# Optimization experiments

Measured on AMD Instinct MI355X. Metric: run time of the kernel, lower is better.

Reference implementation:

```python
import jax, jax.numpy as jnp
import numpy as np
from jax import lax

DILATIONS = (1, 3, 9, 27, 81, 1)
C = 128        # model channels
UP = 2048      # up-projection channels
K = 512        # filterbank kernel size
NZ = 64        # non_zero_elements kept by sparsify
B = 2
N = 32768      # n_samples


def conv1d(x, w, b, dilation=1, padding='VALID'):
    # x: [B,Cin,T], w: [Cout,Cin,Kw]
    y = lax.conv_general_dilated(x, w, (1,), padding, rhs_dilation=(dilation,),
                                 dimension_numbers=('NCH', 'OIH', 'NCH'))
    return y if b is None else y + b[None, :, None]


def dilated_stack(x, ws, bs, causal_past):
    # residual stack of kernel-2 dilated causal convs; 'only-past' pads left, 'only-future' pads right
    for i, d in enumerate(DILATIONS):
        pad = ((0, 0), (0, 0), (d, 0)) if causal_past else ((0, 0), (0, 0), (0, d))
        h = conv1d(jnp.pad(x, pad), ws[i], bs[i], dilation=d)
        x = x + jax.nn.leaky_relu(h, 0.2)
    return x


def sparsify_topk(x, k):
    # keep top-k values (soft=True: keep magnitudes) over flattened (C,T) per sample
    b = x.shape[0]
    flat = x.reshape(b, -1)
    vals, idx = lax.top_k(flat, k)
    out = jnp.zeros_like(flat).at[jnp.arange(b)[:, None], idx].set(vals)
    return out.reshape(x.shape)


def setup_inputs() -> dict:
    key = jax.random.key(0)
    ks = jax.random.split(key, 11)
    s = 0.1  # weight_init
    return {
        'x': jax.random.normal(ks[0], (B, 1, N), jnp.float32),
        'fb': jax.random.normal(ks[1], (C, 1, K), jnp.float32) * s,        # filterbank
        'enc_w': jax.random.normal(ks[2], (6, C, C, 2), jnp.float32) * s,
        'enc_b': jnp.zeros((6, C), jnp.float32),
        'up_w': jax.random.normal(ks[3], (UP, C, 1), jnp.float32) * s,
        'up_b': jnp.zeros((UP,), jnp.float32),
        'down_w': jax.random.normal(ks[4], (C, UP, 1), jnp.float32) * s,
        'down_b': jnp.zeros((C,), jnp.float32),
        'dec_w': jax.random.normal(ks[5], (6, C, C, 2), jnp.float32) * s,
        'dec_b': jnp.zeros((6, C), jnp.float32),
    }


def reference(x, fb, enc_w, enc_b, up_w, up_b, down_w, down_b, dec_w, dec_b):
    # filterbank analysis: [B,1,N] -> [B,C,N]
    spec = conv1d(x, fb, None, 1, ((K // 2, K // 2 - 1),))
    enc = dilated_stack(spec, enc_w, enc_b, causal_past=False)  # 'only-future'
    enc = conv1d(enc, up_w, up_b)            # [B,2048,N]
    enc = sparsify_topk(enc, NZ)             # 64 nonzeros per sample
    enc = conv1d(enc, down_w, down_b)        # [B,128,N]
    dec = dilated_stack(enc, dec_w, dec_b, causal_past=True)    # 'only-past'
    dec = jnp.pad(dec, ((0, 0), (0, 0), (0, 1)))                # F.pad(decoded, (0,1))
    # transposed convolve back to waveform: flipped filterbank, sum over channels
    kt = jnp.flip(fb, -1).transpose(1, 0, 2)  # [1,C,K]
    final = conv1d(dec, kt, None, 1, ((K // 2 - 1, K // 2),))[:, :, :N]
    return final
```

## Files before the change

### kernel.cpp

```cpp
#include <hip/hip_runtime.h>
#include <stdint.h>

#define NB  2
#define NC  128
#define NT  32768
#define KFB 512
#define NUP 2048
#define CAP 14336

typedef unsigned int u32;
typedef unsigned short u16;
typedef short s16;
typedef float f32x4 __attribute__((ext_vector_type(4)));
typedef s16 short8 __attribute__((ext_vector_type(8)));
typedef u32 u32x4 __attribute__((ext_vector_type(4)));

__device__ __forceinline__ u32 f2key(float v){
  u32 u = __float_as_uint(v);
  return (u & 0x80000000u) ? ~u : (u | 0x80000000u);
}
__device__ __forceinline__ float key2f(u32 k){
  u32 u = (k & 0x80000000u) ? (k & 0x7FFFFFFFu) : ~k;
  return __uint_as_float(u);
}
__device__ __forceinline__ u16 bf16rn(float v){
  u32 u = __float_as_uint(v);
  return (u16)((u + 0x7FFFu + ((u>>16)&1u)) >> 16);
}
__device__ __forceinline__ u32 packhl(float v){
  u16 h = bf16rn(v);
  u16 lo = bf16rn(v - __uint_as_float(((u32)h)<<16));
  return ((u32)h<<16) | lo;
}
__device__ __forceinline__ void unpack8(const u32* p, short8& xh, short8& xl){
  u32x4 r0 = *(const u32x4*)p;
  u32x4 r1 = *(const u32x4*)(p + 4);
  union { u32 u[4]; short8 v; } H, L;
  H.u[0] = __builtin_amdgcn_perm(r0.y, r0.x, 0x07060302u);
  H.u[1] = __builtin_amdgcn_perm(r0.w, r0.z, 0x07060302u);
  H.u[2] = __builtin_amdgcn_perm(r1.y, r1.x, 0x07060302u);
  H.u[3] = __builtin_amdgcn_perm(r1.w, r1.z, 0x07060302u);
  L.u[0] = __builtin_amdgcn_perm(r0.y, r0.x, 0x05040100u);
  L.u[1] = __builtin_amdgcn_perm(r0.w, r0.z, 0x05040100u);
  L.u[2] = __builtin_amdgcn_perm(r1.y, r1.x, 0x05040100u);
  L.u[3] = __builtin_amdgcn_perm(r1.w, r1.z, 0x05040100u);
  xh = H.v; xl = L.v;
}

#define RS 132

__global__ __launch_bounds__(256) void k_prep(const float* __restrict__ encw,
    const float* __restrict__ decw, const float* __restrict__ upw,
    const float* __restrict__ fbw,
    u16* __restrict__ wdil, u16* __restrict__ wup, u16* __restrict__ wfb,
    u32* __restrict__ h1, u32* __restrict__ h2, int* __restrict__ counts){
  int g = blockIdx.x*256 + threadIdx.x;
  if (g < 2048) h1[g] = 0u;
  else if (g < 4096) h2[g-2048] = 0u;
  if (g < NB) counts[g] = 0;
  if (g < 49152){
    int l = g & 63, mt = (g>>6)&7, s = (g>>9)&7, layer = g>>12;
    const float* W = (layer < 6) ? (encw + (size_t)layer*NC*NC*2)
                                 : (decw + (size_t)(layer-6)*NC*NC*2);
    int co = mt*16 + (l & 15);
    int kb = s*32 + ((l>>4)<<3);
    union { u16 h[8]; u32x4 q; } H, L;
    #pragma unroll
    for (int j=0;j<8;++j){
      int k = kb + j;
      float v = W[((size_t)co*NC + (k&127))*2 + (k>>7)];
      u16 h = bf16rn(v);
      H.h[j] = h;
      L.h[j] = bf16rn(v - __uint_as_float(((u32)h)<<16));
    }
    int unit = g >> 6;
    *(u32x4*)(wdil + (size_t)unit*1024 + (l<<3)) = H.q;
    *(u32x4*)(wdil + (size_t)unit*1024 + 512 + (l<<3)) = L.q;
  } else if (g < 81920){
    int g2 = g - 49152;
    int l = g2 & 63, umt = (g2>>6)&127, s = g2>>13;
    int u = umt*16 + (l & 15);
    int kb = s*32 + ((l>>4)<<3);
    union { u16 h[8]; u32x4 q; } H, L;
    #pragma unroll
    for (int j=0;j<8;++j){
      float v = upw[(size_t)u*NC + kb + j];
      u16 h = bf16rn(v);
      H.h[j] = h;
      L.h[j] = bf16rn(v - __uint_as_float(((u32)h)<<16));
    }
    int unit = g2 >> 6;
    *(u32x4*)(wup + (size_t)unit*1024 + (l<<3)) = H.q;
    *(u32x4*)(wup + (size_t)unit*1024 + 512 + (l<<3)) = L.q;
  } else if (g < 90112){
    int g3 = g - 81920;
    int l = g3 & 63, mt = (g3>>6)&7, s = g3>>9;
    int c = mt*16 + (l & 15);
    int kb = s*32 + ((l>>4)<<3);
    union { u16 h[8]; u32x4 q; } H, L;
    #pragma unroll
    for (int j=0;j<8;++j){
      float v = fbw[(size_t)c*KFB + kb + j];
      u16 h = bf16rn(v);
      H.h[j] = h;
      L.h[j] = bf16rn(v - __uint_as_float(((u32)h)<<16));
    }
    int unit = g3 >> 6;
    *(u32x4*)(wfb + (size_t)unit*1024 + (l<<3)) = H.q;
    *(u32x4*)(wfb + (size_t)unit*1024 + 512 + (l<<3)) = L.q;
  }
}

__global__ __launch_bounds__(256) void k_fb(const float* __restrict__ x,
    const u16* __restrict__ wfb, float* __restrict__ spec){
  __shared__ u32 xw[640];
  const int tid = threadIdx.x;
  const int t0 = blockIdx.x << 7;
  const int b  = blockIdx.y;
  const int lane = tid & 63, w = tid >> 6;
  const int wy = w >> 1, wx = w & 1;
  const int quad = lane >> 4, l15 = lane & 15;
  for (int i = tid; i < 640; i += 256){
    int t = t0 - 256 + i;
    float v = ((u32)t < (u32)NT) ? x[b*NT + t] : 0.0f;
    xw[i] = packhl(v);
  }
  __syncthreads();
  f32x4 acc[4][4] = {};
  for (int s = 0; s < 16; ++s){
    short8 ah[4], al[4];
    #pragma unroll
    for (int mt=0; mt<4; ++mt){
      const u16* p = wfb + (size_t)(s*8 + wy*4 + mt)*1024 + (lane<<3);
      ah[mt] = *(const short8*)p;
      al[mt] = *(const short8*)(p + 512);
    }
    short8 xh[4], xl[4];
    #pragma unroll
    for (int nt=0; nt<4; ++nt){
      int base = s*32 + quad*8 + (wx<<6) + (nt<<4) + l15;
      u32 r[8];
      #pragma unroll
      for (int j=0;j<8;++j) r[j] = xw[base + j];
      union { u32 u[4]; short8 v; } H, L;
      H.u[0] = __builtin_amdgcn_perm(r[1], r[0], 0x07060302u);
      H.u[1] = __builtin_amdgcn_perm(r[3], r[2], 0x07060302u);
      H.u[2] = __builtin_amdgcn_perm(r[5], r[4], 0x07060302u);
      H.u[3] = __builtin_amdgcn_perm(r[7], r[6], 0x07060302u);
      L.u[0] = __builtin_amdgcn_perm(r[1], r[0], 0x05040100u);
      L.u[1] = __builtin_amdgcn_perm(r[3], r[2], 0x05040100u);
      L.u[2] = __builtin_amdgcn_perm(r[5], r[4], 0x05040100u);
      L.u[3] = __builtin_amdgcn_perm(r[7], r[6], 0x05040100u);
      xh[nt] = H.v; xl[nt] = L.v;
    }
    #pragma unroll
    for (int mt=0; mt<4; ++mt){
      #pragma unroll
      for (int nt=0; nt<4; ++nt){
        acc[mt][nt] = __builtin_amdgcn_mfma_f32_16x16x32_bf16(ah[mt], xh[nt], acc[mt][nt], 0,0,0);
        acc[mt][nt] = __builtin_amdgcn_mfma_f32_16x16x32_bf16(ah[mt], xl[nt], acc[mt][nt], 0,0,0);
        acc[mt][nt] = __builtin_amdgcn_mfma_f32_16x16x32_bf16(al[mt], xh[nt], acc[mt][nt], 0,0,0);
      }
    }
  }
  #pragma unroll
  for (int mt=0; mt<4; ++mt){
    #pragma unroll
    for (int r=0; r<4; ++r){
      const int c = (wy<<6) + (mt<<4) + (quad<<2) + r;
      float* po = spec + (size_t)(b*NC+c)*NT + t0 + (wx<<6) + l15;
      #pragma unroll
      for (int nt=0; nt<4; ++nt) po[nt<<4] = acc[mt][nt][r];
    }
  }
}

__global__ __launch_bounds__(1024,4) void k_stack(const float* __restrict__ xin,
    float* __restrict__ xout, const u16* __restrict__ wf,
    const float* __restrict__ biases, int mode){
  extern __shared__ u32 lx[];
  const int tid = threadIdx.x;
  const int b  = blockIdx.y;
  const int T0 = blockIdx.x << 7;
  const int row0g = mode ? (T0 - 122) : T0;
  const int lane = tid & 63, w = tid >> 6;
  const int wm = w >> 2, wn = w & 3;
  const int quad = lane >> 4, l15 = lane & 15;
  {
    const float* xb = xin + (size_t)b*NC*NT;
    const int row = tid & 255;
    const int ci0 = (tid >> 8) << 5;
    const int tg = row0g + row;
    const bool ok = ((u32)tg < (u32)NT);
    const float* src = xb + (size_t)ci0*NT + tg;
    u32* dst = lx + row*RS + ci0;
    #pragma unroll
    for (int g=0; g<8; ++g){
      u32x4 q;
      #pragma unroll
      for (int k=0;k<4;++k){
        float v = ok ? src[(size_t)(g*4 + k)*NT] : 0.0f;
        q[k] = packhl(v);
      }
      *(u32x4*)(dst + g*4) = q;
    }
  }
  const int dils[6] = {1,3,9,27,81,1};
  const int Hrem[6] = {121,118,109,82,1,0};
  #pragma unroll 1
  for (int l = 0; l < 6; ++l){
    const int d = dils[l];
    const int o0 = mode ? -d : 0;
    const int o1 = mode ? 0 : d;
    const int lo = mode ? (122 - Hrem[l]) : 0;
    const int hi = mode ? 250 : (128 + Hrem[l]);
    const u16* wl = wf + ((size_t)l << 16);
    __syncthreads();
    bool act[4];
    #pragma unroll
    for (int nt=0;nt<4;++nt){
      const int Tst = (wn<<6) + (nt<<4);
      act[nt] = (Tst + 16 > lo) && (Tst < hi);
    }
    f32x4 acc[2][4] = {};
    #pragma unroll 1
    for (int s = 0; s < 8; ++s){
      short8 ah[2], al[2];
      #pragma unroll
      for (int mt=0;mt<2;++mt){
        const u16* p = wl + (size_t)(((s<<3) + (wm<<1) + mt) << 10) + (lane<<3);
        ah[mt] = *(const short8*)p;
        al[mt] = *(const short8*)(p + 512);
      }
      const int o = (s >= 4) ? o1 : o0;
      const int cig = (s & 3) << 5;
      #pragma unroll
      for (int nt=0;nt<4;++nt){
        if (!act[nt]) continue;
        const int T = ((wn<<6) + (nt<<4) + l15 + o) & 255;
        const int idx = T*RS + cig + (quad<<3);
        short8 xh, xl;
        unpack8(&lx[idx], xh, xl);
        #pragma unroll
        for (int mt=0;mt<2;++mt){
          acc[mt][nt] = __builtin_amdgcn_mfma_f32_16x16x32_bf16(ah[mt], xh, acc[mt][nt], 0,0,0);
          acc[mt][nt] = __builtin_amdgcn_mfma_f32_16x16x32_bf16(ah[mt], xl, acc[mt][nt], 0,0,0);
          acc[mt][nt] = __builtin_amdgcn_mfma_f32_16x16x32_bf16(al[mt], xh, acc[mt][nt], 0,0,0);
        }
      }
    }
    __syncthreads();
    const float* bl = biases + l*NC;
    const bool last = (l == 5);
    #pragma unroll
    for (int mt=0;mt<2;++mt){
      const int cobase = (wm<<5) + (mt<<4) + (quad<<2);
      float bv[4];
      #pragma unroll
      for (int r=0;r<4;++r) bv[r] = bl[cobase + r];
      #pragma unroll
      for (int nt=0;nt<4;++nt){
        if (!act[nt]) continue;
        const int T = (wn<<6) + (nt<<4) + l15;
        const int idx = T*RS + cobase;
        u32x4 xo = *(const u32x4*)&lx[idx];
        const int tg = row0g + T;
        const bool tvld = ((u32)tg < (u32)NT);
        float nv[4];
        #pragma unroll
        for (int r=0;r<4;++r){
          float oldv = __uint_as_float(xo[r] & 0xFFFF0000u) + __uint_as_float(xo[r] << 16);
          float h = acc[mt][nt][r] + bv[r];
          h = (h >= 0.f) ? h : 0.2f*h;
          float xn = oldv + h;
          nv[r] = tvld ? xn : 0.0f;
        }
        if (!last){
          u32x4 np;
          #pragma unroll
          for (int r=0;r<4;++r) np[r] = packhl(nv[r]);
          *(u32x4*)&lx[idx] = np;
        } else {
          const bool rowok = mode ? (T >= 122 && T < 250) : (T < 128);
          if (rowok){
            float* po = xout + (size_t)(b*NC + cobase)*NT + tg;
            #pragma unroll
            for (int r=0;r<4;++r) po[(size_t)r*NT] = nv[r];
          }
        }
      }
    }
  }
}

__global__ __launch_bounds__(256) void k_sub(const float* __restrict__ enc,
                                             const float* __restrict__ upw,
                                             const float* __restrict__ upb,
                                             u32* __restrict__ keys,
                                             u32* __restrict__ hist1){
  const int u0 = blockIdx.x * 64;
  const int i0 = blockIdx.y * 256;
  const int b  = blockIdx.z;
  __shared__ float uwl[32][68];
  __shared__ float ec[32][260];
  __shared__ u32 lh[1024];
  const int tid = threadIdx.x;
  for (int i=tid;i<1024;i+=256) lh[i] = 0u;
  const int ug = tid & 15;
  const int ig = tid >> 4;
  float acc[4][16];
  #pragma unroll
  for (int i=0;i<4;++i){
    #pragma unroll
    for (int j=0;j<16;++j) acc[i][j]=0.0f;
  }
  for (int c0=0;c0<NC;c0+=32){
    __syncthreads();
    #pragma unroll
    for (int i=0;i<8;++i){
      int flat = i*256+tid;
      uwl[flat & 31][flat >> 5] = upw[(size_t)(u0 + (flat>>5))*NC + c0 + (flat&31)];
    }
    #pragma unroll
    for (int i=0;i<32;++i){
      int flat = i*256+tid;
      ec[flat >> 8][flat & 255] = enc[(size_t)(b*NC + c0 + (flat>>8))*NT + (size_t)(i0 + (flat&255))*32];
    }
    __syncthreads();
    #pragma unroll 2
    for (int cc=0;cc<32;++cc){
      float a[4], bb[16];
      *(float4*)&a[0] = *(const float4*)&uwl[cc][ug*4];
      #pragma unroll
      for (int m=0;m<4;++m)
        *(float4*)&bb[m*4] = *(const float4*)&ec[cc][ig*16 + m*4];
      #pragma unroll
      for (int i=0;i<4;++i){
        #pragma unroll
        for (int j=0;j<16;++j)
          acc[i][j] = fmaf(a[i], bb[j], acc[i][j]);
      }
    }
  }
  #pragma unroll
  for (int i=0;i<4;++i){
    int u = u0 + ug*4 + i;
    float ub = upb[u];
    #pragma unroll
    for (int j=0;j<16;++j){
      float v = acc[i][j] + ub;
      u32 k = f2key(v);
      keys[(size_t)(b*NUP + u)*1024 + i0 + ig*16 + j] = k;
      atomicAdd(&lh[k >> 22], 1u);
    }
  }
  __syncthreads();
  for (int i=tid;i<1024;i+=256){
    u32 c = lh[i];
    if (c) atomicAdd(&hist1[b*1024 + i], c);
  }
}

__global__ __launch_bounds__(256) void k_sel(const u32* __restrict__ hist,
                                             u32* __restrict__ cstar,
                                             u32* __restrict__ nab,
                                             u32* __restrict__ t0key,
                                             int phase){
  const int b = blockIdx.x;
  __shared__ u32 s1[1024];
  __shared__ u32 s2[1024];
  __shared__ int red[256];
  const int tid = threadIdx.x;
  for (int i=tid;i<1024;i+=256) s1[i] = hist[b*1024 + i];
  __syncthreads();
  u32* cur = s1; u32* nxt = s2;
  for (int off=1; off<1024; off<<=1){
    for (int i=tid;i<1024;i+=256){
      u32 v = cur[i];
      if (i + off < 1024) v += cur[i+off];
      nxt[i] = v;
    }
    __syncthreads();
    u32* t = cur; cur = nxt; nxt = t;
  }
  u32 off0 = (phase==1) ? 0u : nab[b];
  int best = -1;
  for (int i=tid;i<1024;i+=256)
    if (off0 + cur[i] >= 64u && i > best) best = i;
  red[tid] = best;
  __syncthreads();
  for (int st=128; st>0; st>>=1){
    if (tid < st) red[tid] = max(red[tid], red[tid+st]);
    __syncthreads();
  }
  if (tid == 0){
    int bi = (red[0] < 0) ? 0 : red[0];
    if (phase == 1){
      cstar[b] = (u32)bi;
      nab[b] = (bi < 1023) ? cur[bi+1] : 0u;
    } else {
      t0key[b] = (cstar[b] << 22) | (((u32)bi) << 12);
    }
  }
}

__global__ void k_h2(const u32* __restrict__ keys, const u32* __restrict__ cstar,
                     u32* __restrict__ hist2){
  const u32 c0 = cstar[0], c1 = cstar[1];
  int i = blockIdx.x*256 + threadIdx.x;
  const int total = NB*NUP*1024;
  const int stride = gridDim.x*256;
  for (; i < total; i += stride){
    u32 k = keys[i];
    u32 cs = (i >> 21) ? c1 : c0;
    if ((k >> 22) == cs) atomicAdd(&hist2[((u32)(i>>21)<<10) + ((k>>12) & 1023u)], 1u);
  }
}

__global__ __launch_bounds__(256,2) void k_up(const float* __restrict__ enc,
    const u16* __restrict__ wf, const float* __restrict__ upb,
    const u32* __restrict__ t0key, float* __restrict__ cval,
    int* __restrict__ cidx, int* __restrict__ counts){
  extern __shared__ u32 lx[];
  const int tid = threadIdx.x;
  const int t0 = blockIdx.x << 7;
  const int b  = blockIdx.y;
  const int lane = tid & 63, w = tid >> 6;
  const int wy = w >> 1, wx = w & 1;
  const int quad = lane >> 4, l15 = lane & 15;
  {
    const float* xb = enc + (size_t)b*NC*NT + t0;
    const int row = tid >> 1;
    const int ci0 = (tid & 1) << 6;
    const float* src = xb + (size_t)ci0*NT + row;
    u32* dst = lx + row*RS + ci0;
    #pragma unroll
    for (int g=0; g<16; ++g){
      u32x4 q;
      #pragma unroll
      for (int k=0;k<4;++k) q[k] = packhl(src[(size_t)(g*4 + k)*NT]);
      *(u32x4*)(dst + g*4) = q;
    }
  }
  __syncthreads();
  float T0 = key2f(t0key[b]);
  T0 -= fabsf(T0)*3e-4f + 1e-5f;
  #pragma unroll 1
  for (int uc = 0; uc < 16; ++uc){
    f32x4 acc[4][4] = {};
    #pragma unroll 1
    for (int s = 0; s < 4; ++s){
      short8 ah[4], al[4];
      #pragma unroll
      for (int mt=0;mt<4;++mt){
        const u16* p = wf + (size_t)((s*128 + uc*8 + wy*4 + mt) << 10) + (lane<<3);
        ah[mt] = *(const short8*)p;
        al[mt] = *(const short8*)(p + 512);
      }
      const int cig = s << 5;
      #pragma unroll
      for (int nt=0;nt<4;++nt){
        const int T = (wx<<6) + (nt<<4) + l15;
        short8 xh, xl;
        unpack8(&lx[T*RS + cig + (quad<<3)], xh, xl);
        #pragma unroll
        for (int mt=0;mt<4;++mt){
          acc[mt][nt] = __builtin_amdgcn_mfma_f32_16x16x32_bf16(ah[mt], xh, acc[mt][nt], 0,0,0);
          acc[mt][nt] = __builtin_amdgcn_mfma_f32_16x16x32_bf16(ah[mt], xl, acc[mt][nt], 0,0,0);
          acc[mt][nt] = __builtin_amdgcn_mfma_f32_16x16x32_bf16(al[mt], xh, acc[mt][nt], 0,0,0);
        }
      }
    }
    #pragma unroll
    for (int mt=0; mt<4; ++mt){
      #pragma unroll
      for (int r=0; r<4; ++r){
        int u = uc*128 + (wy<<6) + (mt<<4) + (quad<<2) + r;
        float ub = upb[u];
        #pragma unroll
        for (int nt=0; nt<4; ++nt){
          float v = acc[mt][nt][r] + ub;
          if (v >= T0){
            int slot = atomicAdd(&counts[b], 1);
            if (slot < CAP){
              cval[b*CAP + slot] = v;
              cidx[b*CAP + slot] = u*NT + (t0 + (wx<<6) + (nt<<4) + l15);
            }
          }
        }
      }
    }
  }
}

__global__ __launch_bounds__(256) void k_top(const float* __restrict__ cval,
                                             const int* __restrict__ cidx,
                                             const int* __restrict__ counts,
                                             float* __restrict__ tv,
                                             int* __restrict__ ti){
  const int b = blockIdx.x;
  __shared__ float lv[CAP];
  __shared__ float sv[256];
  __shared__ int   si[256];
  const int tid = threadIdx.x;
  int n = counts[b]; if (n > CAP) n = CAP;
  if (n <= 4096){
    float v[16];
    #pragma unroll
    for (int r=0;r<16;++r){
      int i = r*256 + tid;
      v[r] = (i < n) ? cval[b*CAP+i] : -3.4e38f;
    }
    const int lane = tid & 63, wv = tid >> 6;
    for (int r=0;r<64;++r){
      float best = v[0]; int bidx = 0;
      #pragma unroll
      for (int k=1;k<16;++k){ if (v[k] > best){ best = v[k]; bidx = k; } }
      int gi = bidx*256 + tid;
      #pragma unroll
      for (int off=32; off>0; off>>=1){
        float ov = __shfl_down(best, off);
        int oi = __shfl_down(gi, off);
        if (ov > best){ best = ov; gi = oi; }
      }
      if (lane == 0){ sv[wv] = best; si[wv] = gi; }
      __syncthreads();
      if (tid == 0){
        float bb = sv[0]; int bbi = si[0];
        #pragma unroll
        for (int k=1;k<4;++k) if (sv[k] > bb){ bb = sv[k]; bbi = si[k]; }
        si[4] = bbi;
        if (bb > -3.0e38f){ tv[b*64+r] = bb; ti[b*64+r] = cidx[b*CAP + bbi]; }
        else { tv[b*64+r] = 0.0f; ti[b*64+r] = 0; }
      }
      __syncthreads();
      int wini = si[4];
      if ((wini & 255) == tid) v[wini >> 8] = -3.4e38f;
    }
  } else {
    for (int i=tid;i<n;i+=256) lv[i] = cval[b*CAP+i];
    __syncthreads();
    for (int r=0;r<64;++r){
      float best = -3.4e38f; int bi = -1;
      for (int i=tid;i<n;i+=256){
        float v = lv[i];
        if (v > best){ best = v; bi = i; }
      }
      sv[tid]=best; si[tid]=bi;
      __syncthreads();
      for (int st=128; st>0; st>>=1){
        if (tid < st && sv[tid+st] > sv[tid]){ sv[tid]=sv[tid+st]; si[tid]=si[tid+st]; }
        __syncthreads();
      }
      if (tid == 0){
        int kb = si[0];
        if (kb >= 0){
          tv[b*64+r] = sv[0];
          ti[b*64+r] = cidx[b*CAP+kb];
          lv[kb] = -3.4e38f;
        } else { tv[b*64+r] = 0.0f; ti[b*64+r] = 0; }
      }
      __syncthreads();
    }
  }
}

__global__ void k_fill(float* __restrict__ dst, const float* __restrict__ downb){
  const int bc = blockIdx.x;
  const int c = bc & 127;
  float v = downb[c];
  float4 vv; vv.x=v; vv.y=v; vv.z=v; vv.w=v;
  float4* p = (float4*)(dst + (size_t)bc*NT);
  for (int i=threadIdx.x; i < NT/4; i += 256) p[i] = vv;
}

__global__ void k_scat(float* __restrict__ dst, const float* __restrict__ downw,
                       const float* __restrict__ tv, const int* __restrict__ ti){
  const int b = blockIdx.x, r = blockIdx.y;
  float v = tv[b*64+r];
  int idx = ti[b*64+r];
  int u = idx / NT, t = idx - u*NT;
  int c = threadIdx.x;
  atomicAdd(&dst[(size_t)(b*NC+c)*NT + t], downw[(size_t)c*NUP + u] * v);
}

#define TS 4096
__global__ __launch_bounds__(256) void k_syn(const float* __restrict__ dec,
                                             const float* __restrict__ fb,
                                             float* __restrict__ part){
  const int ts = blockIdx.x;
  const int cs = blockIdx.y;
  const int b  = blockIdx.z;
  const int t0 = ts * TS;
  __shared__ float win2[16*289 + 8];
  __shared__ float fbl[512];
  const int tid = threadIdx.x;
  const int tl = tid * 16;
  float acc[16];
  #pragma unroll
  for (int j=0;j<16;++j) acc[j] = 0.0f;
  for (int c = cs*2; c < cs*2+2; ++c){
    __syncthreads();
    for (int i=tid; i < TS+511; i += 256){
      int t = t0 - 255 + i;
      win2[(i & 15)*289 + (i >> 4)] = ((u32)t < (u32)NT) ? dec[(size_t)(b*NC+c)*NT + t] : 0.0f;
    }
    for (int i=tid; i<512; i+=256) fbl[i] = fb[c*KFB + i];
    __syncthreads();
    float w[23];
    #pragma unroll
    for (int k=0;k<23;++k){
      int i = tl + 504 + k;
      w[k] = win2[(i & 15)*289 + (i >> 4)];
    }
    for (int G=0; G<64; ++G){
      float4 f0 = *(const float4*)&fbl[G*8];
      float4 f1 = *(const float4*)&fbl[G*8+4];
      float fq[8] = {f0.x, f0.y, f0.z, f0.w, f1.x, f1.y, f1.z, f1.w};
      #pragma unroll
      for (int q=0;q<8;++q){
        #pragma unroll
        for (int jj=0;jj<16;++jj)
          acc[jj] = fmaf(fq[q], w[7-q+jj], acc[jj]);
      }
      if (G != 63){
        #pragma unroll
        for (int k=22;k>=8;--k) w[k] = w[k-8];
        #pragma unroll
        for (int k=0;k<8;++k){
          int i = tl + 496 - 8*G + k;
          w[k] = win2[(i & 15)*289 + (i >> 4)];
        }
      }
    }
  }
  float* po = &part[(size_t)(cs*NB + b)*NT + t0 + tl];
  #pragma unroll
  for (int m=0;m<4;++m){
    float4 ov; ov.x=acc[m*4+0]; ov.y=acc[m*4+1]; ov.z=acc[m*4+2]; ov.w=acc[m*4+3];
    *(float4*)&po[m*4] = ov;
  }
}

__global__ void k_red(const float* __restrict__ part, float* __restrict__ out){
  int i = blockIdx.x*256 + threadIdx.x;
  float s = 0.0f;
  #pragma unroll
  for (int cs=0;cs<64;++cs) s += part[(size_t)cs*(NB*NT) + i];
  out[i] = s;
}

extern "C" void kernel_launch(void* const* d_in, const int* in_sizes, int n_in,
                              void* d_out, int out_size, void* d_ws, size_t ws_size,
                              hipStream_t stream){
  const float* x    = (const float*)d_in[0];
  const float* fb   = (const float*)d_in[1];
  const float* encw = (const float*)d_in[2];
  const float* encb = (const float*)d_in[3];
  const float* upw  = (const float*)d_in[4];
  const float* upb  = (const float*)d_in[5];
  const float* dnw  = (const float*)d_in[6];
  const float* dnb  = (const float*)d_in[7];
  const float* decw = (const float*)d_in[8];
  const float* decb = (const float*)d_in[9];
  float* out = (float*)d_out;
  char* ws = (char*)d_ws;

  size_t o = 0;
  float* bufA = (float*)(ws + o); o += (size_t)NB*NC*NT*4;
  float* bufB = (float*)(ws + o); o += (size_t)NB*NC*NT*4;
  u32*  keys  = (u32*)(ws + o);   o += (size_t)NB*NUP*1024*4;
  u32*  hist1 = (u32*)(ws + o);   o += 1024*NB*4;
  u32*  hist2 = (u32*)(ws + o);   o += 1024*NB*4;
  u32*  cstar = (u32*)(ws + o);   o += 64;
  u32*  nab   = (u32*)(ws + o);   o += 64;
  u32*  t0k   = (u32*)(ws + o);   o += 64;
  int*  cnt   = (int*)(ws + o);   o += 64;
  float* tv   = (float*)(ws + o); o += NB*64*4;
  int*  ti    = (int*)(ws + o);   o += NB*64*4;
  float* cval = (float*)(ws + o); o += (size_t)NB*CAP*4;
  int*  cidx  = (int*)(ws + o);   o += (size_t)NB*CAP*4;
  u16*  wdil  = (u16*)(ws + o);   o += (size_t)12*65536*2;
  u16*  wup   = (u16*)(ws + o);   o += (size_t)4*128*1024*2;
  u16*  wfb   = (u16*)(ws + o);   o += (size_t)128*1024*2;
  float* part = (float*)keys;

  k_prep<<<dim3(352), dim3(256), 0, stream>>>(encw, decw, upw, fb, wdil, wup, wfb, hist1, hist2, cnt);
  k_fb<<<dim3(256,NB), dim3(256), 0, stream>>>(x, wfb, bufA);

  k_stack<<<dim3(256,NB), dim3(1024), 256*RS*4, stream>>>(bufA, bufB, wdil, encb, 0);

  k_sub<<<dim3(32,4,NB), dim3(256), 0, stream>>>(bufB, upw, upb, keys, hist1);
  k_sel<<<dim3(NB), dim3(256), 0, stream>>>(hist1, cstar, nab, t0k, 1);
  k_h2 <<<dim3(4096), dim3(256), 0, stream>>>(keys, cstar, hist2);
  k_sel<<<dim3(NB), dim3(256), 0, stream>>>(hist2, cstar, nab, t0k, 2);
  k_up <<<dim3(256,NB), dim3(256), 128*RS*4, stream>>>(bufB, wup, upb, t0k, cval, cidx, cnt);
  k_top<<<dim3(NB), dim3(256), 0, stream>>>(cval, cidx, cnt, tv, ti);

  k_fill<<<dim3(NB*NC), dim3(256), 0, stream>>>(bufA, dnb);
  k_scat<<<dim3(NB,64), dim3(128), 0, stream>>>(bufA, dnw, tv, ti);

  k_stack<<<dim3(256,NB), dim3(1024), 256*RS*4, stream>>>(bufA, bufB, wdil + (size_t)6*65536, decb, 1);

  k_syn<<<dim3(8,64,NB), dim3(256), 0, stream>>>(bufB, fb, part);
  k_red<<<dim3(256), dim3(256), 0, stream>>>(part, out);
}
```

Before: 819.5 us.

## Split hi/lo bf16 LDS planes, prefetch weights, fuse fill+scatter, widen synthesis grid

Activations in LDS are now stored as separate hi and lo bf16 planes, so MFMA operands load directly and no longer need perm-based unpacking. The weight fragments for the next k-step are register-prefetched in k_stack and k_up, and k_up's loop is flattened into a single pipelined loop. k_fill and k_scat are merged into one kernel. k_syn now runs one channel per block instead of two, with a float4-vectorised reduction over 128 partials written into bufA. These changes add register pressure and double the size of the partial-sum buffer in exchange for less ALU repacking and more parallelism.

```diff
diff --git a/kernel.cpp b/kernel.cpp
--- a/kernel.cpp
+++ b/kernel.cpp
@@ -14,6 +14,7 @@
 typedef float f32x4 __attribute__((ext_vector_type(4)));
 typedef s16 short8 __attribute__((ext_vector_type(8)));
 typedef u32 u32x4 __attribute__((ext_vector_type(4)));
+typedef u32 u32x2 __attribute__((ext_vector_type(2)));
 
 __device__ __forceinline__ u32 f2key(float v){
   u32 u = __float_as_uint(v);
@@ -32,22 +33,8 @@
   u16 lo = bf16rn(v - __uint_as_float(((u32)h)<<16));
   return ((u32)h<<16) | lo;
 }
-__device__ __forceinline__ void unpack8(const u32* p, short8& xh, short8& xl){
-  u32x4 r0 = *(const u32x4*)p;
-  u32x4 r1 = *(const u32x4*)(p + 4);
-  union { u32 u[4]; short8 v; } H, L;
-  H.u[0] = __builtin_amdgcn_perm(r0.y, r0.x, 0x07060302u);
-  H.u[1] = __builtin_amdgcn_perm(r0.w, r0.z, 0x07060302u);
-  H.u[2] = __builtin_amdgcn_perm(r1.y, r1.x, 0x07060302u);
-  H.u[3] = __builtin_amdgcn_perm(r1.w, r1.z, 0x07060302u);
-  L.u[0] = __builtin_amdgcn_perm(r0.y, r0.x, 0x05040100u);
-  L.u[1] = __builtin_amdgcn_perm(r0.w, r0.z, 0x05040100u);
-  L.u[2] = __builtin_amdgcn_perm(r1.y, r1.x, 0x05040100u);
-  L.u[3] = __builtin_amdgcn_perm(r1.w, r1.z, 0x05040100u);
-  xh = H.v; xl = L.v;
-}
-
-#define RS 132
+
+#define RSH 136
 
 __global__ __launch_bounds__(256) void k_prep(const float* __restrict__ encw,
     const float* __restrict__ decw, const float* __restrict__ upw,
@@ -178,7 +165,9 @@
 __global__ __launch_bounds__(1024,4) void k_stack(const float* __restrict__ xin,
     float* __restrict__ xout, const u16* __restrict__ wf,
     const float* __restrict__ biases, int mode){
-  extern __shared__ u32 lx[];
+  extern __shared__ u16 ls[];
+  u16* lh = ls;
+  u16* ll = ls + 256*RSH;
   const int tid = threadIdx.x;
   const int b  = blockIdx.y;
   const int T0 = blockIdx.x << 7;
@@ -193,16 +182,20 @@
     const int tg = row0g + row;
     const bool ok = ((u32)tg < (u32)NT);
     const float* src = xb + (size_t)ci0*NT + tg;
-    u32* dst = lx + row*RS + ci0;
-    #pragma unroll
-    for (int g=0; g<8; ++g){
-      u32x4 q;
-      #pragma unroll
-      for (int k=0;k<4;++k){
-        float v = ok ? src[(size_t)(g*4 + k)*NT] : 0.0f;
-        q[k] = packhl(v);
-      }
-      *(u32x4*)(dst + g*4) = q;
+    u16* dh = lh + row*RSH + ci0;
+    u16* dl = ll + row*RSH + ci0;
+    #pragma unroll
+    for (int g=0; g<4; ++g){
+      union { u16 h[8]; short8 v; } H, L;
+      #pragma unroll
+      for (int j=0;j<8;++j){
+        float v = ok ? src[(size_t)(g*8 + j)*NT] : 0.0f;
+        u16 hh = bf16rn(v);
+        H.h[j] = hh;
+        L.h[j] = bf16rn(v - __uint_as_float(((u32)hh)<<16));
+      }
+      *(short8*)(dh + (g<<3)) = H.v;
+      *(short8*)(dl + (g<<3)) = L.v;
     }
   }
   const int dils[6] = {1,3,9,27,81,1};
@@ -223,31 +216,38 @@
       act[nt] = (Tst + 16 > lo) && (Tst < hi);
     }
     f32x4 acc[2][4] = {};
+    short8 cah[2], cal[2], nah[2], nal[2];
+    {
+      const u16* p0 = wl + (size_t)(((wm<<1) + 0) << 10) + (lane<<3);
+      const u16* p1 = wl + (size_t)(((wm<<1) + 1) << 10) + (lane<<3);
+      cah[0] = *(const short8*)p0; cal[0] = *(const short8*)(p0 + 512);
+      cah[1] = *(const short8*)p1; cal[1] = *(const short8*)(p1 + 512);
+    }
     #pragma unroll 1
     for (int s = 0; s < 8; ++s){
-      short8 ah[2], al[2];
-      #pragma unroll
-      for (int mt=0;mt<2;++mt){
-        const u16* p = wl + (size_t)(((s<<3) + (wm<<1) + mt) << 10) + (lane<<3);
-        ah[mt] = *(const short8*)p;
-        al[mt] = *(const short8*)(p + 512);
-      }
+      const int sn = (s < 7) ? (s + 1) : 7;
+      const u16* p0 = wl + (size_t)(((sn<<3) + (wm<<1) + 0) << 10) + (lane<<3);
+      const u16* p1 = wl + (size_t)(((sn<<3) + (wm<<1) + 1) << 10) + (lane<<3);
+      nah[0] = *(const short8*)p0; nal[0] = *(const short8*)(p0 + 512);
+      nah[1] = *(const short8*)p1; nal[1] = *(const short8*)(p1 + 512);
       const int o = (s >= 4) ? o1 : o0;
       const int cig = (s & 3) << 5;
       #pragma unroll
       for (int nt=0;nt<4;++nt){
         if (!act[nt]) continue;
         const int T = ((wn<<6) + (nt<<4) + l15 + o) & 255;
-        const int idx = T*RS + cig + (quad<<3);
-        short8 xh, xl;
-        unpack8(&lx[idx], xh, xl);
-        #pragma unroll
-        for (int mt=0;mt<2;++mt){
-          acc[mt][nt] = __builtin_amdgcn_mfma_f32_16x16x32_bf16(ah[mt], xh, acc[mt][nt], 0,0,0);
-          acc[mt][nt] = __builtin_amdgcn_mfma_f32_16x16x32_bf16(ah[mt], xl, acc[mt][nt], 0,0,0);
-          acc[mt][nt] = __builtin_amdgcn_mfma_f32_16x16x32_bf16(al[mt], xh, acc[mt][nt], 0,0,0);
-        }
-      }
+        const int base = T*RSH + cig + (quad<<3);
+        short8 xh = *(const short8*)&lh[base];
+        short8 xl = *(const short8*)&ll[base];
+        acc[0][nt] = __builtin_amdgcn_mfma_f32_16x16x32_bf16(cah[0], xh, acc[0][nt], 0,0,0);
+        acc[0][nt] = __builtin_amdgcn_mfma_f32_16x16x32_bf16(cah[0], xl, acc[0][nt], 0,0,0);
+        acc[0][nt] = __builtin_amdgcn_mfma_f32_16x16x32_bf16(cal[0], xh, acc[0][nt], 0,0,0);
+        acc[1][nt] = __builtin_amdgcn_mfma_f32_16x16x32_bf16(cah[1], xh, acc[1][nt], 0,0,0);
+        acc[1][nt] = __builtin_amdgcn_mfma_f32_16x16x32_bf16(cah[1], xl, acc[1][nt], 0,0,0);
+        acc[1][nt] = __builtin_amdgcn_mfma_f32_16x16x32_bf16(cal[1], xh, acc[1][nt], 0,0,0);
+      }
+      cah[0] = nah[0]; cal[0] = nal[0];
+      cah[1] = nah[1]; cal[1] = nal[1];
     }
     __syncthreads();
     const float* bl = biases + l*NC;
@@ -262,24 +262,30 @@
       for (int nt=0;nt<4;++nt){
         if (!act[nt]) continue;
         const int T = (wn<<6) + (nt<<4) + l15;
-        const int idx = T*RS + cobase;
-        u32x4 xo = *(const u32x4*)&lx[idx];
+        const int base = T*RSH + cobase;
+        union { u16 h[4]; u32x2 q; } HH, LL;
+        HH.q = *(const u32x2*)&lh[base];
+        LL.q = *(const u32x2*)&ll[base];
         const int tg = row0g + T;
         const bool tvld = ((u32)tg < (u32)NT);
         float nv[4];
         #pragma unroll
         for (int r=0;r<4;++r){
-          float oldv = __uint_as_float(xo[r] & 0xFFFF0000u) + __uint_as_float(xo[r] << 16);
+          float oldv = __uint_as_float(((u32)HH.h[r])<<16) + __uint_as_float(((u32)LL.h[r])<<16);
           float h = acc[mt][nt][r] + bv[r];
           h = (h >= 0.f) ? h : 0.2f*h;
           float xn = oldv + h;
           nv[r] = tvld ? xn : 0.0f;
         }
         if (!last){
-          u32x4 np;
           #pragma unroll
-          for (int r=0;r<4;++r) np[r] = packhl(nv[r]);
-          *(u32x4*)&lx[idx] = np;
+          for (int r=0;r<4;++r){
+            u16 hh = bf16rn(nv[r]);
+            HH.h[r] = hh;
+            LL.h[r] = bf16rn(nv[r] - __uint_as_float(((u32)hh)<<16));
+          }
+          *(u32x2*)&lh[base] = HH.q;
+          *(u32x2*)&ll[base] = LL.q;
         } else {
           const bool rowok = mode ? (T >= 122 && T < 250) : (T < 128);
           if (rowok){
@@ -421,7 +427,9 @@
     const u16* __restrict__ wf, const float* __restrict__ upb,
     const u32* __restrict__ t0key, float* __restrict__ cval,
     int* __restrict__ cidx, int* __restrict__ counts){
-  extern __shared__ u32 lx[];
+  extern __shared__ u16 ls[];
+  u16* lh = ls;
+  u16* ll = ls + 128*RSH;
   const int tid = threadIdx.x;
   const int t0 = blockIdx.x << 7;
   const int b  = blockIdx.y;
@@ -433,63 +441,85 @@
     const int row = tid >> 1;
     const int ci0 = (tid & 1) << 6;
     const float* src = xb + (size_t)ci0*NT + row;
-    u32* dst = lx + row*RS + ci0;
-    #pragma unroll
-    for (int g=0; g<16; ++g){
-      u32x4 q;
-      #pragma unroll
-      for (int k=0;k<4;++k) q[k] = packhl(src[(size_t)(g*4 + k)*NT]);
-      *(u32x4*)(dst + g*4) = q;
+    u16* dh = lh + row*RSH + ci0;
+    u16* dl = ll + row*RSH + ci0;
+    #pragma unroll
+    for (int g=0; g<8; ++g){
+      union { u16 h[8]; short8 v; } H, L;
+      #pragma unroll
+      for (int j=0;j<8;++j){
+        float v = src[(size_t)(g*8 + j)*NT];
+        u16 hh = bf16rn(v);
+        H.h[j] = hh;
+        L.h[j] = bf16rn(v - __uint_as_float(((u32)hh)<<16));
+      }
+      *(short8*)(dh + (g<<3)) = H.v;
+      *(short8*)(dl + (g<<3)) = L.v;
     }
   }
   __syncthreads();
   float T0 = key2f(t0key[b]);
   T0 -= fabsf(T0)*3e-4f + 1e-5f;
+  short8 cah[4], cal[4], nah[4], nal[4];
+  {
+    #pragma unroll
+    for (int mt=0;mt<4;++mt){
+      const u16* p = wf + (size_t)((wy*4 + mt) << 10) + (lane<<3);
+      cah[mt] = *(const short8*)p; cal[mt] = *(const short8*)(p + 512);
+    }
+  }
+  f32x4 acc[4][4] = {};
   #pragma unroll 1
-  for (int uc = 0; uc < 16; ++uc){
-    f32x4 acc[4][4] = {};
-    #pragma unroll 1
-    for (int s = 0; s < 4; ++s){
-      short8 ah[4], al[4];
+  for (int ss = 0; ss < 64; ++ss){
+    const int uc = ss >> 2, s = ss & 3;
+    const int ssn = (ss < 63) ? (ss + 1) : 63;
+    const int ucn = ssn >> 2, sn = ssn & 3;
+    #pragma unroll
+    for (int mt=0;mt<4;++mt){
+      const u16* p = wf + (size_t)((sn*128 + ucn*8 + wy*4 + mt) << 10) + (lane<<3);
+      nah[mt] = *(const short8*)p; nal[mt] = *(const short8*)(p + 512);
+    }
+    const int cig = s << 5;
+    #pragma unroll
+    for (int nt=0;nt<4;++nt){
+      const int T = (wx<<6) + (nt<<4) + l15;
+      const int base = T*RSH + cig + (quad<<3);
+      short8 xh = *(const short8*)&lh[base];
+      short8 xl = *(const short8*)&ll[base];
       #pragma unroll
       for (int mt=0;mt<4;++mt){
-        const u16* p = wf + (size_t)((s*128 + uc*8 + wy*4 + mt) << 10) + (lane<<3);
-        ah[mt] = *(const short8*)p;
-        al[mt] = *(const short8*)(p + 512);
-      }
-      const int cig = s << 5;
-      #pragma unroll
-      for (int nt=0;nt<4;++nt){
-        const int T = (wx<<6) + (nt<<4) + l15;
-        short8 xh, xl;
-        unpack8(&lx[T*RS + cig + (quad<<3)], xh, xl);
+        acc[mt][nt] = __builtin_amdgcn_mfma_f32_16x16x32_bf16(cah[mt], xh, acc[mt][nt], 0,0,0);
+        acc[mt][nt] = __builtin_amdgcn_mfma_f32_16x16x32_bf16(cah[mt], xl, acc[mt][nt], 0,0,0);
+        acc[mt][nt] = __builtin_amdgcn_mfma_f32_16x16x32_bf16(cal[mt], xh, acc[mt][nt], 0,0,0);
+      }
+    }
+    if (s == 3){
+      #pragma unroll
+      for (int mt=0; mt<4; ++mt){
         #pragma unroll
-        for (int mt=0;mt<4;++mt){
-          acc[mt][nt] = __builtin_amdgcn_mfma_f32_16x16x32_bf16(ah[mt], xh, acc[mt][nt], 0,0,0);
-          acc[mt][nt] = __builtin_amdgcn_mfma_f32_16x16x32_bf16(ah[mt], xl, acc[mt][nt], 0,0,0);
-          acc[mt][nt] = __builtin_amdgcn_mfma_f32_16x16x32_bf16(al[mt], xh, acc[mt][nt], 0,0,0);
-        }
-      }
-    }
-    #pragma unroll
-    for (int mt=0; mt<4; ++mt){
-      #pragma unroll
-      for (int r=0; r<4; ++r){
-        int u = uc*128 + (wy<<6) + (mt<<4) + (quad<<2) + r;
-        float ub = upb[u];
-        #pragma unroll
-        for (int nt=0; nt<4; ++nt){
-          float v = acc[mt][nt][r] + ub;
-          if (v >= T0){
-            int slot = atomicAdd(&counts[b], 1);
-            if (slot < CAP){
-              cval[b*CAP + slot] = v;
-              cidx[b*CAP + slot] = u*NT + (t0 + (wx<<6) + (nt<<4) + l15);
+        for (int r=0; r<4; ++r){
+          int u = uc*128 + (wy<<6) + (mt<<4) + (quad<<2) + r;
+          float ub = upb[u];
+          #pragma unroll
+          for (int nt=0; nt<4; ++nt){
+            float v = acc[mt][nt][r] + ub;
+            if (v >= T0){
+              int slot = atomicAdd(&counts[b], 1);
+              if (slot < CAP){
+                cval[b*CAP + slot] = v;
+                cidx[b*CAP + slot] = u*NT + (t0 + (wx<<6) + (nt<<4) + l15);
+              }
             }
           }
         }
       }
-    }
+      #pragma unroll
+      for (int mt=0;mt<4;++mt)
+        #pragma unroll
+        for (int nt=0;nt<4;++nt) acc[mt][nt] = (f32x4){0.f,0.f,0.f,0.f};
+    }
+    #pragma unroll
+    for (int mt=0;mt<4;++mt){ cah[mt] = nah[mt]; cal[mt] = nal[mt]; }
   }
 }
 
@@ -565,23 +595,22 @@
   }
 }
 
-__global__ void k_fill(float* __restrict__ dst, const float* __restrict__ downb){
-  const int bc = blockIdx.x;
-  const int c = bc & 127;
-  float v = downb[c];
+__global__ void k_dec0(float* __restrict__ dst, const float* __restrict__ dnb,
+                       const float* __restrict__ dnw,
+                       const float* __restrict__ tv, const int* __restrict__ ti){
+  const int b = blockIdx.x >> 7, c = blockIdx.x & 127;
+  float v = dnb[c];
   float4 vv; vv.x=v; vv.y=v; vv.z=v; vv.w=v;
-  float4* p = (float4*)(dst + (size_t)bc*NT);
-  for (int i=threadIdx.x; i < NT/4; i += 256) p[i] = vv;
-}
-
-__global__ void k_scat(float* __restrict__ dst, const float* __restrict__ downw,
-                       const float* __restrict__ tv, const int* __restrict__ ti){
-  const int b = blockIdx.x, r = blockIdx.y;
-  float v = tv[b*64+r];
-  int idx = ti[b*64+r];
-  int u = idx / NT, t = idx - u*NT;
-  int c = threadIdx.x;
-  atomicAdd(&dst[(size_t)(b*NC+c)*NT + t], downw[(size_t)c*NUP + u] * v);
+  float* row = dst + (size_t)(b*NC+c)*NT;
+  for (int i=threadIdx.x; i < NT/4; i += 256) *(float4*)&row[i*4] = vv;
+  __syncthreads();
+  if (threadIdx.x < 64){
+    int r = threadIdx.x;
+    float sv = tv[b*64+r];
+    int idx = ti[b*64+r];
+    int u = idx / NT, t = idx - u*NT;
+    atomicAdd(&row[t], dnw[(size_t)c*NUP + u] * sv);
+  }
 }
 
 #define TS 4096
@@ -589,7 +618,7 @@
                                              const float* __restrict__ fb,
                                              float* __restrict__ part){
   const int ts = blockIdx.x;
-  const int cs = blockIdx.y;
+  const int c  = blockIdx.y;
   const int b  = blockIdx.z;
   const int t0 = ts * TS;
   __shared__ float win2[16*289 + 8];
@@ -599,42 +628,39 @@
   float acc[16];
   #pragma unroll
   for (int j=0;j<16;++j) acc[j] = 0.0f;
-  for (int c = cs*2; c < cs*2+2; ++c){
-    __syncthreads();
-    for (int i=tid; i < TS+511; i += 256){
-      int t = t0 - 255 + i;
-      win2[(i & 15)*289 + (i >> 4)] = ((u32)t < (u32)NT) ? dec[(size_t)(b*NC+c)*NT + t] : 0.0f;
-    }
-    for (int i=tid; i<512; i+=256) fbl[i] = fb[c*KFB + i];
-    __syncthreads();
-    float w[23];
-    #pragma unroll
-    for (int k=0;k<23;++k){
-      int i = tl + 504 + k;
-      w[k] = win2[(i & 15)*289 + (i >> 4)];
-    }
-    for (int G=0; G<64; ++G){
-      float4 f0 = *(const float4*)&fbl[G*8];
-      float4 f1 = *(const float4*)&fbl[G*8+4];
-      float fq[8] = {f0.x, f0.y, f0.z, f0.w, f1.x, f1.y, f1.z, f1.w};
-      #pragma unroll
-      for (int q=0;q<8;++q){
-        #pragma unroll
-        for (int jj=0;jj<16;++jj)
-          acc[jj] = fmaf(fq[q], w[7-q+jj], acc[jj]);
-      }
-      if (G != 63){
-        #pragma unroll
-        for (int k=22;k>=8;--k) w[k] = w[k-8];
-        #pragma unroll
-        for (int k=0;k<8;++k){
-          int i = tl + 496 - 8*G + k;
-          w[k] = win2[(i & 15)*289 + (i >> 4)];
-        }
-      }
-    }
-  }
-  float* po = &part[(size_t)(cs*NB + b)*NT + t0 + tl];
+  for (int i=tid; i < TS+511; i += 256){
+    int t = t0 - 255 + i;
+    win2[(i & 15)*289 + (i >> 4)] = ((u32)t < (u32)NT) ? dec[(size_t)(b*NC+c)*NT + t] : 0.0f;
+  }
+  for (int i=tid; i<512; i+=256) fbl[i] = fb[c*KFB + i];
+  __syncthreads();
+  float w[23];
+  #pragma unroll
+  for (int k=0;k<23;++k){
+    int i = tl + 504 + k;
+    w[k] = win2[(i & 15)*289 + (i >> 4)];
+  }
+  for (int G=0; G<64; ++G){
+    float4 f0 = *(const float4*)&fbl[G*8];
+    float4 f1 = *(const float4*)&fbl[G*8+4];
+    float fq[8] = {f0.x, f0.y, f0.z, f0.w, f1.x, f1.y, f1.z, f1.w};
+    #pragma unroll
+    for (int q=0;q<8;++q){
+      #pragma unroll
+      for (int jj=0;jj<16;++jj)
+        acc[jj] = fmaf(fq[q], w[7-q+jj], acc[jj]);
+    }
+    if (G != 63){
+      #pragma unroll
+      for (int k=22;k>=8;--k) w[k] = w[k-8];
+      #pragma unroll
+      for (int k=0;k<8;++k){
+        int i = tl + 496 - 8*G + k;
+        w[k] = win2[(i & 15)*289 + (i >> 4)];
+      }
+    }
+  }
+  float* po = &part[(size_t)(c*NB + b)*NT + t0 + tl];
   #pragma unroll
   for (int m=0;m<4;++m){
     float4 ov; ov.x=acc[m*4+0]; ov.y=acc[m*4+1]; ov.z=acc[m*4+2]; ov.w=acc[m*4+3];
@@ -643,11 +669,14 @@
 }
 
 __global__ void k_red(const float* __restrict__ part, float* __restrict__ out){
-  int i = blockIdx.x*256 + threadIdx.x;
-  float s = 0.0f;
-  #pragma unroll
-  for (int cs=0;cs<64;++cs) s += part[(size_t)cs*(NB*NT) + i];
-  out[i] = s;
+  int i4 = blockIdx.x*256 + threadIdx.x;
+  float4 s; s.x=0.f; s.y=0.f; s.z=0.f; s.w=0.f;
+  #pragma unroll 4
+  for (int c=0;c<128;++c){
+    float4 p = *(const float4*)&part[(size_t)c*(NB*NT) + (size_t)i4*4];
+    s.x += p.x; s.y += p.y; s.z += p.z; s.w += p.w;
+  }
+  *(float4*)&out[(size_t)i4*4] = s;
 }
 
 extern "C" void kernel_launch(void* const* d_in, const int* in_sizes, int n_in,
@@ -683,25 +712,24 @@
   u16*  wdil  = (u16*)(ws + o);   o += (size_t)12*65536*2;
   u16*  wup   = (u16*)(ws + o);   o += (size_t)4*128*1024*2;
   u16*  wfb   = (u16*)(ws + o);   o += (size_t)128*1024*2;
-  float* part = (float*)keys;
+  float* part = bufA;
 
   k_prep<<<dim3(352), dim3(256), 0, stream>>>(encw, decw, upw, fb, wdil, wup, wfb, hist1, hist2, cnt);
   k_fb<<<dim3(256,NB), dim3(256), 0, stream>>>(x, wfb, bufA);
 
-  k_stack<<<dim3(256,NB), dim3(1024), 256*RS*4, stream>>>(bufA, bufB, wdil, encb, 0);
+  k_stack<<<dim3(256,NB), dim3(1024), 2*256*RSH*2, stream>>>(bufA, bufB, wdil, encb, 0);
 
   k_sub<<<dim3(32,4,NB), dim3(256), 0, stream>>>(bufB, upw, upb, keys, hist1);
   k_sel<<<dim3(NB), dim3(256), 0, stream>>>(hist1, cstar, nab, t0k, 1);
   k_h2 <<<dim3(4096), dim3(256), 0, stream>>>(keys, cstar, hist2);
   k_sel<<<dim3(NB), dim3(256), 0, stream>>>(hist2, cstar, nab, t0k, 2);
-  k_up <<<dim3(256,NB), dim3(256), 128*RS*4, stream>>>(bufB, wup, upb, t0k, cval, cidx, cnt);
+  k_up <<<dim3(256,NB), dim3(256), 2*128*RSH*2, stream>>>(bufB, wup, upb, t0k, cval, cidx, cnt);
   k_top<<<dim3(NB), dim3(256), 0, stream>>>(cval, cidx, cnt, tv, ti);
 
-  k_fill<<<dim3(NB*NC), dim3(256), 0, stream>>>(bufA, dnb);
-  k_scat<<<dim3(NB,64), dim3(128), 0, stream>>>(bufA, dnw, tv, ti);
-
-  k_stack<<<dim3(256,NB), dim3(1024), 256*RS*4, stream>>>(bufA, bufB, wdil + (size_t)6*65536, decb, 1);
-
-  k_syn<<<dim3(8,64,NB), dim3(256), 0, stream>>>(bufB, fb, part);
-  k_red<<<dim3(256), dim3(256), 0, stream>>>(part, out);
-}
+  k_dec0<<<dim3(NB*NC), dim3(256), 0, stream>>>(bufA, dnb, dnw, tv, ti);
+
+  k_stack<<<dim3(256,NB), dim3(1024), 2*256*RSH*2, stream>>>(bufA, bufB, wdil + (size_t)6*65536, decb, 1);
+
+  k_syn<<<dim3(8,128,NB), dim3(256), 0, stream>>>(bufB, fb, part);
+  k_red<<<dim3(64), dim3(256), 0, stream>>>(part, out);
+}
```

Result: no change. 821.7 us (+0.3%).
